# Kernel optimization log

Hardware: AMD Instinct MI355X
Metric: run time of the kernel (lower is better)

The kernel has to match this reference:

```python
import jax, jax.numpy as jnp
import numpy as np
from jax import lax

MAXW = 4  # spans cover j in [i, min(i+4, max_len)) -> widths 1..4


def setup_inputs() -> dict:
    key = jax.random.key(0)
    ks = jax.random.split(key, 8)
    B, L, H = 64, 512, 256
    Hd = H // 2  # dynamicLSTM hidden = kernel_num/2
    s = 0.05
    feats = jax.random.normal(ks[0], (B, L, H), dtype=jnp.float32)
    lens = jax.random.randint(ks[1], (B,), 1, L + 1)
    W_ih = jax.random.normal(ks[2], (4 * Hd, H), dtype=jnp.float32) * s
    W_hh = jax.random.normal(ks[3], (4 * Hd, Hd), dtype=jnp.float32) * s
    b_ih = jax.random.normal(ks[4], (4 * Hd,), dtype=jnp.float32) * s
    b_hh = jax.random.normal(ks[5], (4 * Hd,), dtype=jnp.float32) * s
    W_tri = jax.random.normal(ks[6], (2, Hd), dtype=jnp.float32) * s
    b_tri = jax.random.normal(ks[7], (2,), dtype=jnp.float32) * s
    return {"feats": feats, "W_ih": W_ih, "W_hh": W_hh, "b_ih": b_ih,
            "b_hh": b_hh, "W_tri": W_tri, "b_tri": b_tri, "lens": lens}


def _build_tag_graph(feats, W_ih, W_hh, b_ih, b_hh, W_tri, b_tri, lens):
    B, Lmax, H = feats.shape
    Hd = W_hh.shape[1]
    starts = jnp.arange(Lmax)
    idx = starts[:, None] + jnp.arange(MAXW)[None, :]              # (L, 4)
    in_range = idx < Lmax
    win = feats[:, jnp.minimum(idx, Lmax - 1)] * in_range[None, :, :, None]  # (B, L, 4, H)
    x = win.transpose(2, 0, 1, 3).reshape(MAXW, B * Lmax, H)       # steps-major

    def step(carry, xt):
        h, c = carry
        gates = xt @ W_ih.T + b_ih + h @ W_hh.T + b_hh
        i_, f_, g_, o_ = jnp.split(gates, 4, axis=-1)  # torch gate order i,f,g,o
        c = jax.nn.sigmoid(f_) * c + jax.nn.sigmoid(i_) * jnp.tanh(g_)
        h = jax.nn.sigmoid(o_) * jnp.tanh(c)
        return (h, c), h

    h0 = jnp.zeros((B * Lmax, Hd), feats.dtype)
    _, hs = lax.scan(step, (h0, h0), x)                            # (4, B*L, Hd)
    hs = hs.reshape(MAXW, B, Lmax, Hd).transpose(1, 2, 0, 3)       # (B, L, 4, Hd); [...,t,:] = hidden after t+1 steps

    # effective packed length per span: total = clip(lens - i, 0, w); pack uses max(total, 1)
    w = jnp.arange(1, MAXW + 1)                                    # span widths
    rem = lens[:, None] - starts[None, :]                          # (B, L)
    total = jnp.clip(rem[:, :, None], 0, w[None, None, :])         # (B, L, 4)
    Lsel = jnp.maximum(total, 1)
    row_mask = (total > 0).astype(feats.dtype)
    h_span = jnp.take_along_axis(hs, (Lsel - 1)[..., None], axis=2)  # (B, L, 4, Hd)

    emit = (h_span @ W_tri.T + b_tri) * row_mask[..., None]        # (B, L, 4, 2)
    # scatter emit[b, i, w-1] into span_scores[b, i, i+w-1]; drop spans past max_len
    valid_span = in_range  # j = i + (w-1) < Lmax
    emit = emit * valid_span[None, :, :, None]
    j_clamped = jnp.minimum(idx, Lmax - 1)
    span_scores = jnp.zeros((B, Lmax, Lmax, 2), feats.dtype)
    span_scores = span_scores.at[:, starts[:, None], j_clamped].add(emit)
    return span_scores


def reference(feats, W_ih, W_hh, b_ih, b_hh, W_tri, b_tri, lens):
    return _build_tag_graph(feats, W_ih, W_hh, b_ih, b_hh, W_tri, b_tri, lens)
```

## Files before the change

### kernel.cpp

```cpp
#include <hip/hip_runtime.h>
#include <cstddef>

#define NB 64
#define LL 512
#define HH 256
#define HD 128
#define NG 512
#define TI 16

typedef _Float16 half_t;
typedef _Float16 half8 __attribute__((ext_vector_type(8)));
typedef _Float16 half4 __attribute__((ext_vector_type(4)));
typedef float f32x4 __attribute__((ext_vector_type(4)));

#define MFMA16(a, b, c) __builtin_amdgcn_mfma_f32_16x16x32_f16((a), (b), (c), 0, 0, 0)

#define FP 264
#define XP 518
#define HBP 136
#define EP 17

__device__ __forceinline__ float sigm(float x)  { return __builtin_amdgcn_rcpf(1.0f + __expf(-x)); }
__device__ __forceinline__ float tanhf_(float x){ return 2.0f * __builtin_amdgcn_rcpf(1.0f + __expf(-2.0f * x)) - 1.0f; }

template <int CTRL>
__device__ __forceinline__ float dppadd(float x) {
    int v = __builtin_amdgcn_update_dpp(0, __float_as_int(x), CTRL, 0xF, 0xF, true);
    return x + __int_as_float(v);
}
__device__ __forceinline__ float row16_sum(float x) {
    x = dppadd<0xB1>(x);
    x = dppadd<0x4E>(x);
    x = dppadd<0x141>(x);
    x = dppadd<0x140>(x);
    return x;
}

__global__ void prep_weights(const float* __restrict__ Wih, const float* __restrict__ Whh,
                             const float* __restrict__ bih, const float* __restrict__ bhh,
                             half_t* __restrict__ WihH, half_t* __restrict__ WhhH,
                             float* __restrict__ bsum)
{
    const int idx = blockIdx.x * 256 + threadIdx.x;
    if (idx < NG * HH) WihH[idx] = (half_t)Wih[idx];
    if (idx < NG * HD) WhhH[idx] = (half_t)Whh[idx];
    if (idx < NG)      bsum[idx] = bih[idx] + bhh[idx];
}

__global__ __launch_bounds__(512, 4) void span_lstm_mfma(
    const float* __restrict__ feats, const half_t* __restrict__ WihH,
    const half_t* __restrict__ WhhH, const float* __restrict__ bsum,
    const float* __restrict__ W_tri, const float* __restrict__ b_tri,
    const int* __restrict__ lens, float* __restrict__ out)
{
    __shared__ __align__(16) half_t sFeatb[20 * FP];
    __shared__ __align__(16) float  sXG[20 * XP];
    __shared__ __align__(16) half_t sHb[2][16 * HBP];
    __shared__ __align__(16) float  sE[4][16 * EP];

    float* sVal = (float*)sFeatb;

    const int tid = threadIdx.x;
    const int b  = blockIdx.x >> 5;
    const int i0 = (blockIdx.x & 31) * TI;
    const int lens_b = lens[b];

    float* ob = out + ((size_t)b * LL + i0) * (LL * 2);

    if (i0 >= lens_b) {
        f32x4* ob4 = (f32x4*)ob;
        const f32x4 zz = {0.f, 0.f, 0.f, 0.f};
        #pragma unroll
        for (int k = 0; k < 8; ++k)
            ob4[k * 512 + tid] = zz;
        return;
    }

    const int lane = tid & 63, wv = tid >> 6;
    const int lm = lane & 15;
    const int lq = lane >> 4;
    const int jw = wv * 16;

    for (int idx = tid; idx < 20 * 64; idx += 512) {
        const int p  = idx >> 6;
        const int k4 = (idx & 63) << 2;
        const int gp = i0 + p;
        float4 v = make_float4(0.f, 0.f, 0.f, 0.f);
        if (gp < LL) v = *(const float4*)(feats + ((size_t)b * LL + gp) * HH + k4);
        half4 hv = {(half_t)v.x, (half_t)v.y, (half_t)v.z, (half_t)v.w};
        *(half4*)(&sFeatb[p * FP + k4]) = hv;
    }
    __syncthreads();

    {
        half8 afr[2][8];
        #pragma unroll
        for (int mt = 0; mt < 2; ++mt)
            #pragma unroll
            for (int kf = 0; kf < 8; ++kf)
                afr[mt][kf] = *(const half8*)(&sFeatb[(16 * mt + lm) * FP + kf * 32 + lq * 8]);

        #pragma unroll
        for (int ta = 0; ta < 4; ++ta) {
            const int gb = ta * HD + jw;
            const float bs = bsum[gb + lm];
            f32x4 acc0 = {0.f, 0.f, 0.f, 0.f}, acc1 = {0.f, 0.f, 0.f, 0.f};
            #pragma unroll
            for (int kf = 0; kf < 8; ++kf) {
                const half8 bfr = *(const half8*)(WihH + (size_t)(gb + lm) * HH + kf * 32 + lq * 8);
                acc0 = MFMA16(afr[0][kf], bfr, acc0);
                acc1 = MFMA16(afr[1][kf], bfr, acc1);
            }
            #pragma unroll
            for (int r = 0; r < 4; ++r)
                sXG[(lq * 4 + r) * XP + gb + lm] = acc0[r] + bs;
            if (lq == 0) {
                #pragma unroll
                for (int r = 0; r < 4; ++r)
                    sXG[(16 + r) * XP + gb + lm] = acc1[r] + bs;
            }
        }
    }

    half8 bf2[4][4];
    #pragma unroll
    for (int ta = 0; ta < 4; ++ta)
        #pragma unroll
        for (int kf = 0; kf < 4; ++kf)
            bf2[ta][kf] = *(const half8*)(WhhH + (size_t)(ta * HD + jw + lm) * HD
                                          + kf * 32 + lq * 8);

    float cc4[4]   = {0.f, 0.f, 0.f, 0.f};
    float hhA[4][4];

    #pragma unroll
    for (int t = 0; t < 4; ++t) {
        float accg[4][4];
        if (t > 0) {
            half8 ah[4];
            #pragma unroll
            for (int kf = 0; kf < 4; ++kf)
                ah[kf] = *(const half8*)(&sHb[(t - 1) & 1][lm * HBP + kf * 32 + lq * 8]);
            #pragma unroll
            for (int ta = 0; ta < 4; ++ta) {
                f32x4 a = {0.f, 0.f, 0.f, 0.f};
                #pragma unroll
                for (int kf = 0; kf < 4; ++kf)
                    a = MFMA16(ah[kf], bf2[ta][kf], a);
                #pragma unroll
                for (int r = 0; r < 4; ++r) accg[ta][r] = a[r];
            }
        } else {
            #pragma unroll
            for (int ta = 0; ta < 4; ++ta)
                #pragma unroll
                for (int r = 0; r < 4; ++r) accg[ta][r] = 0.f;
        }
        #pragma unroll
        for (int ta = 0; ta < 4; ++ta)
            #pragma unroll
            for (int r = 0; r < 4; ++r)
                accg[ta][r] += sXG[(lq * 4 + r + t) * XP + ta * HD + jw + lm];

        #pragma unroll
        for (int r = 0; r < 4; ++r) {
            const float ig = sigm(accg[0][r]);
            const float fg = sigm(accg[1][r]);
            const float gg = tanhf_(accg[2][r]);
            const float og = sigm(accg[3][r]);
            cc4[r] = fg * cc4[r] + ig * gg;
            hhA[t][r] = og * tanhf_(cc4[r]);
        }

        if (t < 3) {
            #pragma unroll
            for (int r = 0; r < 4; ++r)
                sHb[t & 1][(lq * 4 + r) * HBP + jw + lm] = (half_t)hhA[t][r];
            __syncthreads();
        }
    }

    {
        const float wt0 = W_tri[jw + lm];
        const float wt1 = W_tri[HD + jw + lm];
        #pragma unroll
        for (int ts = 0; ts < 4; ++ts)
            #pragma unroll
            for (int r = 0; r < 4; ++r) {
                float e0 = row16_sum(hhA[ts][r] * wt0);
                float e1 = row16_sum(hhA[ts][r] * wt1);
                if (lm == 0) {
                    float2 v = make_float2(e0, e1);
                    *(float2*)&sE[ts][(lq * 4 + r) * EP + wv * 2] = v;
                }
            }
    }
    __syncthreads();

    if (tid < 128) {
        const int es = tid & 15, tag = (tid >> 4) & 1, w = (tid >> 5) + 1;
        const int i = i0 + es;
        const int rem = lens_b - i;
        float e = 0.f;
        if (rem > 0 && (i + w - 1) < LL) {
            const int ts = (rem < w ? rem : w) - 1;
            e = b_tri[tag];
            #pragma unroll
            for (int k = 0; k < 8; ++k) e += sE[ts][es * EP + k * 2 + tag];
        }
        sVal[(es * 4 + (w - 1)) * 2 + tag] = e;
    }
    __syncthreads();

    #pragma unroll
    for (int k = 0; k < 8; ++k) {
        const int cg = k * 512 + tid;
        const int es = cg >> 8;
        const int c  = cg & 255;
        const int jlo = 2 * c;
        const int i  = i0 + es;
        f32x4 v = {0.f, 0.f, 0.f, 0.f};
        const int w0 = jlo - i + 1;
        if ((unsigned)(w0 - 1) < 4u) {
            v.x = sVal[(es * 4 + (w0 - 1)) * 2 + 0];
            v.y = sVal[(es * 4 + (w0 - 1)) * 2 + 1];
        }
        const int w1 = w0 + 1;
        if ((unsigned)(w1 - 1) < 4u) {
            v.z = sVal[(es * 4 + (w1 - 1)) * 2 + 0];
            v.w = sVal[(es * 4 + (w1 - 1)) * 2 + 1];
        }
        *(f32x4*)(ob + (size_t)cg * 4) = v;
    }
}

extern "C" void kernel_launch(void* const* d_in, const int* in_sizes, int n_in,
                              void* d_out, int out_size, void* d_ws, size_t ws_size,
                              hipStream_t stream)
{
    const float* feats = (const float*)d_in[0];
    const float* W_ih  = (const float*)d_in[1];
    const float* W_hh  = (const float*)d_in[2];
    const float* b_ih  = (const float*)d_in[3];
    const float* b_hh  = (const float*)d_in[4];
    const float* W_tri = (const float*)d_in[5];
    const float* b_tri = (const float*)d_in[6];
    const int*   lens  = (const int*)d_in[7];
    float* out = (float*)d_out;


    half_t* WihH = (half_t*)d_ws;
    half_t* WhhH = WihH + (size_t)NG * HH;
    float*  bsum = (float*)(WhhH + (size_t)NG * HD);

    prep_weights<<<(NG * HH + 255) / 256, 256, 0, stream>>>(W_ih, W_hh, b_ih, b_hh,
                                                            WihH, WhhH, bsum);
    span_lstm_mfma<<<NB * (LL / TI), 512, 0, stream>>>(feats, WihH, WhhH, bsum,
                                                       W_tri, b_tri, lens, out);
}
```

Before: 251.4 us.

## Issue zero stores before LSTM recurrence and write only nonzero span band at end

Moves the bulk of the zero output writes (all columns outside each row's span band) ahead of the LSTM recurrence, using nontemporal stores so they overlap with compute. The final epilogue then writes only the up to three 16-byte chunks per row that can hold span scores. It also swaps __syncthreads for a raw LDS-wait plus s_barrier and hoists the W_tri/b_tri loads earlier. The aim is to hide the large output write traffic behind MFMA work, at the cost of more complex partitioning logic and register pressure from the early stores.

New measurement: 266.1 us. +5.8%, slower.

```diff
diff --git a/kernel.cpp b/kernel.cpp
--- a/kernel.cpp
+++ b/kernel.cpp
@@ -34,6 +34,12 @@
     x = dppadd<0x141>(x);
     x = dppadd<0x140>(x);
     return x;
+}
+
+__device__ __forceinline__ void barrier_lgkm() {
+    asm volatile("s_waitcnt lgkmcnt(0)" ::: "memory");
+    __builtin_amdgcn_s_barrier();
+    asm volatile("" ::: "memory");
 }
 
 __global__ void prep_weights(const float* __restrict__ Wih, const float* __restrict__ Whh,
@@ -66,13 +72,12 @@
     const int lens_b = lens[b];
 
     float* ob = out + ((size_t)b * LL + i0) * (LL * 2);
+    const f32x4 zz = {0.f, 0.f, 0.f, 0.f};
 
     if (i0 >= lens_b) {
-        f32x4* ob4 = (f32x4*)ob;
-        const f32x4 zz = {0.f, 0.f, 0.f, 0.f};
         #pragma unroll
         for (int k = 0; k < 8; ++k)
-            ob4[k * 512 + tid] = zz;
+            __builtin_nontemporal_store(zz, (f32x4*)(ob + (size_t)(k * 512 + tid) * 4));
         return;
     }
 
@@ -129,8 +134,32 @@
         for (int kf = 0; kf < 4; ++kf)
             bf2[ta][kf] = *(const half8*)(WhhH + (size_t)(ta * HD + jw + lm) * HD
                                           + kf * 32 + lq * 8);
-
-    float cc4[4]   = {0.f, 0.f, 0.f, 0.f};
+    const float wt0 = W_tri[jw + lm];
+    const float wt1 = W_tri[HD + jw + lm];
+    const float bt0 = b_tri[0], bt1 = b_tri[1];
+
+    asm volatile("" :: "v"(wt0), "v"(wt1), "v"(bt0), "v"(bt1));
+    #pragma unroll
+    for (int ta = 0; ta < 4; ++ta)
+        #pragma unroll
+        for (int kf = 0; kf < 4; ++kf)
+            asm volatile("" :: "v"(bf2[ta][kf]));
+
+    #pragma unroll
+    for (int k = 0; k < 8; ++k) {
+        const int cg = k * 512 + tid;
+        const int es = cg >> 8, c = cg & 255;
+        const int i  = i0 + es;
+        bool mixed = false;
+        if (i < lens_b) {
+            const int chi = ((i + 3 < LL) ? (i + 3) : (LL - 1)) >> 1;
+            mixed = (c >= (i >> 1)) && (c <= chi);
+        }
+        if (!mixed)
+            __builtin_nontemporal_store(zz, (f32x4*)(ob + (size_t)cg * 4));
+    }
+
+    float cc4[4] = {0.f, 0.f, 0.f, 0.f};
     float hhA[4][4];
 
     #pragma unroll
@@ -176,26 +205,22 @@
             #pragma unroll
             for (int r = 0; r < 4; ++r)
                 sHb[t & 1][(lq * 4 + r) * HBP + jw + lm] = (half_t)hhA[t][r];
-            __syncthreads();
-        }
-    }
-
-    {
-        const float wt0 = W_tri[jw + lm];
-        const float wt1 = W_tri[HD + jw + lm];
-        #pragma unroll
-        for (int ts = 0; ts < 4; ++ts)
-            #pragma unroll
-            for (int r = 0; r < 4; ++r) {
-                float e0 = row16_sum(hhA[ts][r] * wt0);
-                float e1 = row16_sum(hhA[ts][r] * wt1);
-                if (lm == 0) {
-                    float2 v = make_float2(e0, e1);
-                    *(float2*)&sE[ts][(lq * 4 + r) * EP + wv * 2] = v;
-                }
-            }
-    }
-    __syncthreads();
+            barrier_lgkm();
+        }
+    }
+
+    #pragma unroll
+    for (int ts = 0; ts < 4; ++ts)
+        #pragma unroll
+        for (int r = 0; r < 4; ++r) {
+            float e0 = row16_sum(hhA[ts][r] * wt0);
+            float e1 = row16_sum(hhA[ts][r] * wt1);
+            if (lm == 0) {
+                float2 v = make_float2(e0, e1);
+                *(float2*)&sE[ts][(lq * 4 + r) * EP + wv * 2] = v;
+            }
+        }
+    barrier_lgkm();
 
     if (tid < 128) {
         const int es = tid & 15, tag = (tid >> 4) & 1, w = (tid >> 5) + 1;
@@ -204,33 +229,36 @@
         float e = 0.f;
         if (rem > 0 && (i + w - 1) < LL) {
             const int ts = (rem < w ? rem : w) - 1;
-            e = b_tri[tag];
+            e = tag ? bt1 : bt0;
             #pragma unroll
             for (int k = 0; k < 8; ++k) e += sE[ts][es * EP + k * 2 + tag];
         }
         sVal[(es * 4 + (w - 1)) * 2 + tag] = e;
     }
-    __syncthreads();
-
-    #pragma unroll
-    for (int k = 0; k < 8; ++k) {
-        const int cg = k * 512 + tid;
-        const int es = cg >> 8;
-        const int c  = cg & 255;
-        const int jlo = 2 * c;
-        const int i  = i0 + es;
-        f32x4 v = {0.f, 0.f, 0.f, 0.f};
-        const int w0 = jlo - i + 1;
-        if ((unsigned)(w0 - 1) < 4u) {
-            v.x = sVal[(es * 4 + (w0 - 1)) * 2 + 0];
-            v.y = sVal[(es * 4 + (w0 - 1)) * 2 + 1];
-        }
-        const int w1 = w0 + 1;
-        if ((unsigned)(w1 - 1) < 4u) {
-            v.z = sVal[(es * 4 + (w1 - 1)) * 2 + 0];
-            v.w = sVal[(es * 4 + (w1 - 1)) * 2 + 1];
-        }
-        *(f32x4*)(ob + (size_t)cg * 4) = v;
+    barrier_lgkm();
+
+    if (tid < 48) {
+        const int es = tid & 15, m = tid >> 4;
+        const int i = i0 + es;
+        if (i < lens_b) {
+            const int chi = ((i + 3 < LL) ? (i + 3) : (LL - 1)) >> 1;
+            const int c = (i >> 1) + m;
+            if (c <= chi) {
+                const int j0 = 2 * c;
+                f32x4 v = {0.f, 0.f, 0.f, 0.f};
+                const int w0 = j0 - i + 1;
+                if ((unsigned)(w0 - 1) < 4u) {
+                    v.x = sVal[(es * 4 + (w0 - 1)) * 2 + 0];
+                    v.y = sVal[(es * 4 + (w0 - 1)) * 2 + 1];
+                }
+                const int w1 = w0 + 1;
+                if ((unsigned)(w1 - 1) < 4u) {
+                    v.z = sVal[(es * 4 + (w1 - 1)) * 2 + 0];
+                    v.w = sVal[(es * 4 + (w1 - 1)) * 2 + 1];
+                }
+                *(f32x4*)(ob + ((size_t)es * 256 + c) * 4) = v;
+            }
+        }
     }
 }
 
@@ -248,7 +276,6 @@
     const int*   lens  = (const int*)d_in[7];
     float* out = (float*)d_out;
 
-
     half_t* WihH = (half_t*)d_ws;
     half_t* WhhH = WihH + (size_t)NG * HH;
     float*  bsum = (float*)(WhhH + (size_t)NG * HD);
```
